# Performance work log

Hardware: AMD Instinct MI355X
Metric: run time of the kernel (lower is better)

Reference implementation:

```python
import jax, jax.numpy as jnp
import numpy as np

PATCH = 15  # box-filter kernel size (odd -> SAME padding == padding=PATCH//2, stride 1)


def _box_filter(x, k):
    """All-ones kxk conv2d, stride 1, zero pad k//2. x: (N,1,H,W).
    The ones kernel is separable: ones(k,k) = ones(k,1) @ ones(1,k)."""
    dn = ('NCHW', 'OIHW', 'NCHW')
    kh = jnp.ones((1, 1, k, 1), x.dtype)
    kw = jnp.ones((1, 1, 1, k), x.dtype)
    x = jax.lax.conv_general_dilated(x, kh, (1, 1), 'SAME', dimension_numbers=dn)
    x = jax.lax.conv_general_dilated(x, kw, (1, 1), 'SAME', dimension_numbers=dn)
    return x


def _rgb_to_yuv420(rgb):
    """rgb: (N,3,H,W) -> y:(N,H,W), u,v:(N,H/2,W/2) (2x2 avg-pooled chroma)."""
    r, g, b = rgb[:, 0], rgb[:, 1], rgb[:, 2]
    y = 0.299 * r + 0.587 * g + 0.114 * b
    u = -0.169 * r - 0.331 * g + 0.5 * b + 128.0
    v = 0.5 * r - 0.46 * g - 0.04 * b + 128.0
    n, h, w = u.shape
    u = u.reshape(n, h // 2, 2, w // 2, 2).mean(axis=(2, 4))
    v = v.reshape(n, h // 2, 2, w // 2, 2).mean(axis=(2, 4))
    return y, u, v


def _filtered_channels(img, k):
    y, u, v = _rgb_to_yuv420(img)
    return (_box_filter(y[:, None], k),
            _box_filter(u[:, None], k),
            _box_filter(v[:, None], k))


def setup_inputs() -> dict:
    key = jax.random.key(0)
    k1, k2 = jax.random.split(key)
    input_ = jax.random.uniform(k1, (16, 3, 512, 512), dtype=jnp.float32)
    target = jax.random.uniform(k2, (16, 3, 512, 512), dtype=jnp.float32)
    return {"input": input_, "target": target}


def reference(input, target):
    yi, ui, vi = _filtered_channels(input, PATCH)
    yt, ut, vt = _filtered_channels(target, PATCH)
    mse = lambda a, b: jnp.mean((a - b) ** 2)
    return mse(yi, yt) + mse(ui, ut) + mse(vi, vt)
```

## Files before the change

kernel.cpp:

```cpp
#include <hip/hip_runtime.h>

#define NIMG 16
#define H 512
#define W 512

__global__ __launch_bounds__(256, 4) void fused_wave_kernel(
        const float* __restrict__ in, const float* __restrict__ tgt,
        float invY, float invC, float* __restrict__ partials) {
    __shared__ float part[4];

    const int tid = threadIdx.x;
    const int wv  = tid >> 6;
    const int l   = tid & 63;

    const int g     = (blockIdx.x & 7) * 128 + (blockIdx.x >> 3);
    const int n     = g >> 6;
    const int band  = (g >> 2) & 15;
    const int strip = ((g & 3) << 2) | wv;

    const size_t plane = (size_t)H * W;
    const float* pi = in  + (size_t)n * 3 * plane;
    const float* pt = tgt + (size_t)n * 3 * plane;

    const int x  = (strip << 5) - 16 + l;
    const int xm = x < 0 ? 0 : (x > W - 1 ? W - 1 : x);
    const float mx = (x == xm) ? 1.f : 0.f;
    const float mL = (l >= 16 && l < 48) ? 1.f : 0.f;

    const bool ev = (l & 1) == 0;
    const float kr = ev ? -0.169f : 0.5f;
    const float kg = ev ? -0.331f : -0.46f;
    const float kb = ev ? 0.5f    : -0.04f;

    const int yBase = (band << 5) - 14;

    float ringA[8], ringB[8], ringC[16];
#pragma unroll
    for (int i = 0; i < 8; ++i) { ringA[i] = 0.f; ringB[i] = 0.f; }
#pragma unroll
    for (int i = 0; i < 16; ++i) ringC[i] = 0.f;

    float V = 0.f, Vc = 0.f, accY = 0.f, accC = 0.f;

#define PAIR(q) do {                                                          \
    const int yA = yBase + 2*(q), yB = yA + 1;                                \
    const int yAc = yA < 0 ? 0 : (yA > H-1 ? H-1 : yA);                       \
    const int yBc = yB < 0 ? 0 : (yB > H-1 ? H-1 : yB);                       \
    const float mA = (yA == yAc) ? mx : 0.f;                                  \
    const float mB = (yB == yBc) ? mx : 0.f;                                  \
    const size_t oA = (size_t)yAc * W + xm;                                   \
    const size_t oB = (size_t)yBc * W + xm;                                   \
    const float irA = pi[oA], igA = pi[plane+oA], ibA = pi[2*plane+oA];       \
    const float trA = pt[oA], tgA = pt[plane+oA], tbA = pt[2*plane+oA];       \
    const float irB = pi[oB], igB = pi[plane+oB], ibB = pi[2*plane+oB];       \
    const float trB = pt[oB], tgB = pt[plane+oB], tbB = pt[2*plane+oB];       \
    const float drA = (irA-trA)*mA, dgA = (igA-tgA)*mA, dbA = (ibA-tbA)*mA;   \
    const float drB = (irB-trB)*mB, dgB = (igB-tgB)*mB, dbB = (ibB-tbB)*mB;   \
    const float dYA = 0.299f*drA + 0.587f*dgA + 0.114f*dbA;                   \
    const float dYB = 0.299f*drB + 0.587f*dgB + 0.114f*dbB;                   \
    const float Va = V + dYA - ringB[(q) & 7];           \
    const float Vb = Va + dYB - ringA[((q)+1) & 7];      \
    ringA[(q) & 7] = dYA;                                                     \
    ringB[(q) & 7] = dYB;                                                     \
    V = Vb;                                                                   \
    if ((q) >= 10 && (q) <= 26) {             \
        float PA = Va, PB = Vb;                                               \
        _Pragma("unroll")                                                     \
        for (int d = 1; d <= 32; d <<= 1) {                                   \
            const float tA = __shfl_up(PA, d, 64);                            \
            const float tB = __shfl_up(PB, d, 64);                            \
            PA += (l >= d) ? tA : 0.f;                                        \
            PB += (l >= d) ? tB : 0.f;                                        \
        }                                                                     \
        const float hA = __shfl_down(PA, 7, 64) - __shfl_up(PA, 8, 64);       \
        const float hB = __shfl_down(PB, 7, 64) - __shfl_up(PB, 8, 64);       \
        if ((q) >= 11) accY += hA * hA * mL;        \
        if ((q) <= 25) accY += hB * hB * mL;        \
    }                                                                         \
    const float hr = drA + drB, hg = dgA + dgB, hb = dbA + dbB;               \
    const float sr = hr + __shfl_xor(hr, 1, 64);                              \
    const float sg = hg + __shfl_xor(hg, 1, 64);                              \
    const float sb = hb + __shfl_xor(hb, 1, 64);                              \
    const float Qc = (kr*sr + kg*sg + kb*sb) * 0.25f;                         \
    Vc += Qc - ringC[((q)+1) & 15];                                           \
    ringC[(q) & 15] = Qc;                                                     \
    if ((q) >= 14 && (q) <= 29) {                \
        float PC = Vc;                                                        \
        _Pragma("unroll")                                                     \
        for (int d = 2; d <= 32; d <<= 1) {                                   \
            const float tC = __shfl_up(PC, d, 64);                            \
            PC += (l >= d) ? tC : 0.f;                                        \
        }                                                                     \
        const float hc = __shfl_down(PC, 14, 64) - __shfl_up(PC, 16, 64);     \
        accC += hc * hc * mL;                                                 \
    }                                                                         \
} while (0)

    PAIR(0);  PAIR(1);  PAIR(2);  PAIR(3);  PAIR(4);  PAIR(5);
    PAIR(6);  PAIR(7);  PAIR(8);  PAIR(9);  PAIR(10); PAIR(11);
    PAIR(12); PAIR(13); PAIR(14); PAIR(15); PAIR(16); PAIR(17);
    PAIR(18); PAIR(19); PAIR(20); PAIR(21); PAIR(22); PAIR(23);
    PAIR(24); PAIR(25); PAIR(26); PAIR(27); PAIR(28); PAIR(29);
#undef PAIR

    float v = accY * invY + accC * invC;
    for (int o = 32; o > 0; o >>= 1) v += __shfl_down(v, o, 64);
    if (l == 0) part[wv] = v;
    __syncthreads();
    if (tid == 0)
        partials[blockIdx.x] = (part[0] + part[1]) + (part[2] + part[3]);
}

__global__ void final_reduce_kernel(const float* __restrict__ partials, int n,
                                    float* __restrict__ out) {
    float s = 0.f;
    for (int i = threadIdx.x; i < n; i += 256) s += partials[i];
    for (int o = 32; o > 0; o >>= 1) s += __shfl_down(s, o, 64);
    __shared__ float part[4];
    const int lane = threadIdx.x & 63, wid = threadIdx.x >> 6;
    if (lane == 0) part[wid] = s;
    __syncthreads();
    if (threadIdx.x == 0)
        *out = part[0] + part[1] + part[2] + part[3];
}

extern "C" void kernel_launch(void* const* d_in, const int* in_sizes, int n_in,
                              void* d_out, int out_size, void* d_ws, size_t ws_size,
                              hipStream_t stream) {
    const float* input  = (const float*)d_in[0];
    const float* target = (const float*)d_in[1];
    float* out = (float*)d_out;
    float* partials = (float*)d_ws;

    const float invY = 1.0f / (float)((size_t)NIMG * H * W);
    const float invC = 1.0f / (float)((size_t)NIMG * (H/2) * (W/2));

    fused_wave_kernel<<<1024, 256, 0, stream>>>(input, target, invY, invC, partials);
    final_reduce_kernel<<<1, 256, 0, stream>>>(partials, 1024, out);
}
```

Before: 139.9 us.

## Process two columns per lane with float2 loads, DPP scans and software prefetch

Each lane now handles two adjacent columns using float2 loads, so each wave covers a 64-column strip with less halo overhead, and the grid shrinks from 1024 to 512 blocks. The shuffle-based prefix scans are replaced with DPP row-shift scans plus ds_bpermute window extraction. Chroma is computed per lane directly from the pixel pair rather than through an xor shuffle. Loads for the next row pair are double-buffered ahead of consumption to hide memory latency. The cost is higher register pressure (launch bounds lowered to 2 blocks per CU) and half as many blocks, which may reduce occupancy.

```diff
diff --git a/kernel.cpp b/kernel.cpp
--- a/kernel.cpp
+++ b/kernel.cpp
@@ -4,7 +4,109 @@
 #define H 512
 #define W 512
 
-__global__ __launch_bounds__(256, 4) void fused_wave_kernel(
+
+template<int CTRL, int RM>
+static __device__ __forceinline__ float dppadd(float v) {
+    return v + __uint_as_float((unsigned)__builtin_amdgcn_update_dpp(
+        0, (int)__float_as_uint(v), CTRL, RM, 0xF, true));
+}
+
+static __device__ __forceinline__ float scan64(float v) {
+    v = dppadd<0x111, 0xF>(v);
+    v = dppadd<0x112, 0xF>(v);
+    v = dppadd<0x114, 0xF>(v);
+    v = dppadd<0x118, 0xF>(v);
+    v = dppadd<0x142, 0xA>(v);
+    v = dppadd<0x143, 0xC>(v);
+    return v;
+}
+
+static __device__ __forceinline__ float bpermf(int byteaddr, float v) {
+    return __uint_as_float((unsigned)__builtin_amdgcn_ds_bpermute(
+        byteaddr, (int)__float_as_uint(v)));
+}
+
+#define LOADP(q, S) do {                                                     \
+    const int yA_ = yBase + 2*(q);                                           \
+    const int yB_ = yA_ + 1;                                                 \
+    const int yAc_ = yA_ < 0 ? 0 : (yA_ > H-1 ? H-1 : yA_);                  \
+    const int yBc_ = yB_ < 0 ? 0 : (yB_ > H-1 ? H-1 : yB_);                  \
+    const size_t oA_ = (size_t)yAc_ * W + xcl;                               \
+    const size_t oB_ = (size_t)yBc_ * W + xcl;                               \
+    S##_0  = *(const float2*)(pi + oA_);                                     \
+    S##_1  = *(const float2*)(pi + plane + oA_);                             \
+    S##_2  = *(const float2*)(pi + 2*plane + oA_);                           \
+    S##_3  = *(const float2*)(pt + oA_);                                     \
+    S##_4  = *(const float2*)(pt + plane + oA_);                             \
+    S##_5  = *(const float2*)(pt + 2*plane + oA_);                           \
+    S##_6  = *(const float2*)(pi + oB_);                                     \
+    S##_7  = *(const float2*)(pi + plane + oB_);                             \
+    S##_8  = *(const float2*)(pi + 2*plane + oB_);                           \
+    S##_9  = *(const float2*)(pt + oB_);                                     \
+    S##_10 = *(const float2*)(pt + plane + oB_);                             \
+    S##_11 = *(const float2*)(pt + 2*plane + oB_);                           \
+} while (0)
+
+#define CONS(q, S) do {                                                      \
+    const int yA_ = yBase + 2*(q);                                           \
+    const float mA_ = ((unsigned)yA_       < (unsigned)H) ? mx : 0.f;        \
+    const float mB_ = ((unsigned)(yA_ + 1) < (unsigned)H) ? mx : 0.f;        \
+    const float drA0_ = (S##_0.x - S##_3.x) * mA_;                           \
+    const float drA1_ = (S##_0.y - S##_3.y) * mA_;                           \
+    const float dgA0_ = (S##_1.x - S##_4.x) * mA_;                           \
+    const float dgA1_ = (S##_1.y - S##_4.y) * mA_;                           \
+    const float dbA0_ = (S##_2.x - S##_5.x) * mA_;                           \
+    const float dbA1_ = (S##_2.y - S##_5.y) * mA_;                           \
+    const float drB0_ = (S##_6.x - S##_9.x) * mB_;                           \
+    const float drB1_ = (S##_6.y - S##_9.y) * mB_;                           \
+    const float dgB0_ = (S##_7.x - S##_10.x) * mB_;                          \
+    const float dgB1_ = (S##_7.y - S##_10.y) * mB_;                          \
+    const float dbB0_ = (S##_8.x - S##_11.x) * mB_;                          \
+    const float dbB1_ = (S##_8.y - S##_11.y) * mB_;                          \
+    const float dYA0_ = 0.299f*drA0_ + 0.587f*dgA0_ + 0.114f*dbA0_;          \
+    const float dYA1_ = 0.299f*drA1_ + 0.587f*dgA1_ + 0.114f*dbA1_;          \
+    const float dYB0_ = 0.299f*drB0_ + 0.587f*dgB0_ + 0.114f*dbB0_;          \
+    const float dYB1_ = 0.299f*drB1_ + 0.587f*dgB1_ + 0.114f*dbB1_;          \
+                    \
+    const float sr_ = (drA0_ + drA1_) + (drB0_ + drB1_);                     \
+    const float sg_ = (dgA0_ + dgA1_) + (dgB0_ + dgB1_);                     \
+    const float sb_ = (dbA0_ + dbA1_) + (dbB0_ + dbB1_);                     \
+    const float u_ = (-0.169f*sr_ - 0.331f*sg_ + 0.5f *sb_) * 0.25f;         \
+    const float w_ = ( 0.5f  *sr_ - 0.46f *sg_ - 0.04f*sb_) * 0.25f;         \
+         \
+    const float VA0_ = V0 + dYA0_ - rB0[(q) & 7];                            \
+    const float VB0_ = VA0_ + dYB0_ - rA0[((q)+1) & 7];                      \
+    rA0[(q) & 7] = dYA0_;  rB0[(q) & 7] = dYB0_;  V0 = VB0_;                 \
+    const float VA1_ = V1 + dYA1_ - rB1[(q) & 7];                            \
+    const float VB1_ = VA1_ + dYB1_ - rA1[((q)+1) & 7];                      \
+    rA1[(q) & 7] = dYA1_;  rB1[(q) & 7] = dYB1_;  V1 = VB1_;                 \
+    const float VU_ = CU + u_ - rU[((q)+1) & 15];                            \
+    rU[(q) & 15] = u_;  CU = VU_;                                            \
+    const float VV_ = CV + w_ - rV[((q)+1) & 15];                            \
+    rV[(q) & 15] = w_;  CV = VV_;                                            \
+        \
+    if ((q) >= 11 && (q) <= 26) {         \
+        const float SA_ = scan64(VA0_ + VA1_);                               \
+        const float h0_ = SA_ - VA1_ - bpermf(am8, SA_);                     \
+        const float h1_ = h0_ + VA1_ - bpermf(am7, VA0_);                    \
+        accY += (h0_ * h0_) * mH0 + (h1_ * h1_) * mH1;                       \
+    }                                                                        \
+    if ((q) >= 10 && (q) <= 25) {         \
+        const float SB_ = scan64(VB0_ + VB1_);                               \
+        const float h0_ = SB_ - VB1_ - bpermf(am8, SB_);                     \
+        const float h1_ = h0_ + VB1_ - bpermf(am7, VB0_);                    \
+        accY += (h0_ * h0_) * mH0 + (h1_ * h1_) * mH1;                       \
+    }                                                                        \
+    if ((q) >= 14) {                    \
+        const float SU_ = scan64(VU_);                                       \
+        const float hU_ = SU_ - bpermf(am15, SU_);                           \
+        const float SV_ = scan64(VV_);                                       \
+        const float hV_ = SV_ - bpermf(am15, SV_);                           \
+        accC += (hU_ * hU_ + hV_ * hV_) * mC;                                \
+    }                                                                        \
+} while (0)
+
+__global__ __launch_bounds__(256, 2) void fused_wave_kernel(
         const float* __restrict__ in, const float* __restrict__ tgt,
         float invY, float invC, float* __restrict__ partials) {
     __shared__ float part[4];
@@ -13,95 +115,59 @@
     const int wv  = tid >> 6;
     const int l   = tid & 63;
 
-    const int g     = (blockIdx.x & 7) * 128 + (blockIdx.x >> 3);
-    const int n     = g >> 6;
-    const int band  = (g >> 2) & 15;
-    const int strip = ((g & 3) << 2) | wv;
+    const int g     = (blockIdx.x & 7) * 64 + (blockIdx.x >> 3);
+    const int n     = g >> 5;
+    const int band  = (g >> 1) & 15;
+    const int strip = ((g & 1) << 2) | wv;
 
     const size_t plane = (size_t)H * W;
     const float* pi = in  + (size_t)n * 3 * plane;
     const float* pt = tgt + (size_t)n * 3 * plane;
 
-    const int x  = (strip << 5) - 16 + l;
-    const int xm = x < 0 ? 0 : (x > W - 1 ? W - 1 : x);
-    const float mx = (x == xm) ? 1.f : 0.f;
-    const float mL = (l >= 16 && l < 48) ? 1.f : 0.f;
-
-    const bool ev = (l & 1) == 0;
-    const float kr = ev ? -0.169f : 0.5f;
-    const float kg = ev ? -0.331f : -0.46f;
-    const float kb = ev ? 0.5f    : -0.04f;
-
-    const int yBase = (band << 5) - 14;
-
-    float ringA[8], ringB[8], ringC[16];
+    const int R0 = band << 5;
+    const int yBase = R0 - 14;
+
+    const int x0 = (strip << 6) - 32 + 2 * l;
+    const int xcl = x0 < 0 ? 0 : (x0 > W - 2 ? W - 2 : x0);
+    const float mx = (x0 == xcl) ? 1.f : 0.f;
+
+    const float mH0 = (l >= 20 && l <= 51) ? 1.f : 0.f;
+    const float mH1 = (l >= 19 && l <= 50) ? 1.f : 0.f;
+    const float mC  = (l >= 23 && l <= 54) ? 1.f : 0.f;
+
+    const int am8  = (l - 8)  << 2;
+    const int am7  = (l - 7)  << 2;
+    const int am15 = (l - 15) << 2;
+
+    float rA0[8], rA1[8], rB0[8], rB1[8], rU[16], rV[16];
 #pragma unroll
-    for (int i = 0; i < 8; ++i) { ringA[i] = 0.f; ringB[i] = 0.f; }
+    for (int i = 0; i < 8; ++i) { rA0[i] = 0.f; rA1[i] = 0.f; rB0[i] = 0.f; rB1[i] = 0.f; }
 #pragma unroll
-    for (int i = 0; i < 16; ++i) ringC[i] = 0.f;
-
-    float V = 0.f, Vc = 0.f, accY = 0.f, accC = 0.f;
-
-#define PAIR(q) do {                                                          \
-    const int yA = yBase + 2*(q), yB = yA + 1;                                \
-    const int yAc = yA < 0 ? 0 : (yA > H-1 ? H-1 : yA);                       \
-    const int yBc = yB < 0 ? 0 : (yB > H-1 ? H-1 : yB);                       \
-    const float mA = (yA == yAc) ? mx : 0.f;                                  \
-    const float mB = (yB == yBc) ? mx : 0.f;                                  \
-    const size_t oA = (size_t)yAc * W + xm;                                   \
-    const size_t oB = (size_t)yBc * W + xm;                                   \
-    const float irA = pi[oA], igA = pi[plane+oA], ibA = pi[2*plane+oA];       \
-    const float trA = pt[oA], tgA = pt[plane+oA], tbA = pt[2*plane+oA];       \
-    const float irB = pi[oB], igB = pi[plane+oB], ibB = pi[2*plane+oB];       \
-    const float trB = pt[oB], tgB = pt[plane+oB], tbB = pt[2*plane+oB];       \
-    const float drA = (irA-trA)*mA, dgA = (igA-tgA)*mA, dbA = (ibA-tbA)*mA;   \
-    const float drB = (irB-trB)*mB, dgB = (igB-tgB)*mB, dbB = (ibB-tbB)*mB;   \
-    const float dYA = 0.299f*drA + 0.587f*dgA + 0.114f*dbA;                   \
-    const float dYB = 0.299f*drB + 0.587f*dgB + 0.114f*dbB;                   \
-    const float Va = V + dYA - ringB[(q) & 7];           \
-    const float Vb = Va + dYB - ringA[((q)+1) & 7];      \
-    ringA[(q) & 7] = dYA;                                                     \
-    ringB[(q) & 7] = dYB;                                                     \
-    V = Vb;                                                                   \
-    if ((q) >= 10 && (q) <= 26) {             \
-        float PA = Va, PB = Vb;                                               \
-        _Pragma("unroll")                                                     \
-        for (int d = 1; d <= 32; d <<= 1) {                                   \
-            const float tA = __shfl_up(PA, d, 64);                            \
-            const float tB = __shfl_up(PB, d, 64);                            \
-            PA += (l >= d) ? tA : 0.f;                                        \
-            PB += (l >= d) ? tB : 0.f;                                        \
-        }                                                                     \
-        const float hA = __shfl_down(PA, 7, 64) - __shfl_up(PA, 8, 64);       \
-        const float hB = __shfl_down(PB, 7, 64) - __shfl_up(PB, 8, 64);       \
-        if ((q) >= 11) accY += hA * hA * mL;        \
-        if ((q) <= 25) accY += hB * hB * mL;        \
-    }                                                                         \
-    const float hr = drA + drB, hg = dgA + dgB, hb = dbA + dbB;               \
-    const float sr = hr + __shfl_xor(hr, 1, 64);                              \
-    const float sg = hg + __shfl_xor(hg, 1, 64);                              \
-    const float sb = hb + __shfl_xor(hb, 1, 64);                              \
-    const float Qc = (kr*sr + kg*sg + kb*sb) * 0.25f;                         \
-    Vc += Qc - ringC[((q)+1) & 15];                                           \
-    ringC[(q) & 15] = Qc;                                                     \
-    if ((q) >= 14 && (q) <= 29) {                \
-        float PC = Vc;                                                        \
-        _Pragma("unroll")                                                     \
-        for (int d = 2; d <= 32; d <<= 1) {                                   \
-            const float tC = __shfl_up(PC, d, 64);                            \
-            PC += (l >= d) ? tC : 0.f;                                        \
-        }                                                                     \
-        const float hc = __shfl_down(PC, 14, 64) - __shfl_up(PC, 16, 64);     \
-        accC += hc * hc * mL;                                                 \
-    }                                                                         \
-} while (0)
-
-    PAIR(0);  PAIR(1);  PAIR(2);  PAIR(3);  PAIR(4);  PAIR(5);
-    PAIR(6);  PAIR(7);  PAIR(8);  PAIR(9);  PAIR(10); PAIR(11);
-    PAIR(12); PAIR(13); PAIR(14); PAIR(15); PAIR(16); PAIR(17);
-    PAIR(18); PAIR(19); PAIR(20); PAIR(21); PAIR(22); PAIR(23);
-    PAIR(24); PAIR(25); PAIR(26); PAIR(27); PAIR(28); PAIR(29);
-#undef PAIR
+    for (int i = 0; i < 16; ++i) { rU[i] = 0.f; rV[i] = 0.f; }
+
+    float V0 = 0.f, V1 = 0.f, CU = 0.f, CV = 0.f;
+    float accY = 0.f, accC = 0.f;
+
+    float2 A_0,A_1,A_2,A_3,A_4,A_5,A_6,A_7,A_8,A_9,A_10,A_11;
+    float2 B_0,B_1,B_2,B_3,B_4,B_5,B_6,B_7,B_8,B_9,B_10,B_11;
+
+    LOADP(0, A);
+    LOADP(1, B);
+    CONS(0, A);  LOADP(2, A);   CONS(1, B);  LOADP(3, B);
+    CONS(2, A);  LOADP(4, A);   CONS(3, B);  LOADP(5, B);
+    CONS(4, A);  LOADP(6, A);   CONS(5, B);  LOADP(7, B);
+    CONS(6, A);  LOADP(8, A);   CONS(7, B);  LOADP(9, B);
+    CONS(8, A);  LOADP(10, A);  CONS(9, B);  LOADP(11, B);
+    CONS(10, A); LOADP(12, A);  CONS(11, B); LOADP(13, B);
+    CONS(12, A); LOADP(14, A);  CONS(13, B); LOADP(15, B);
+    CONS(14, A); LOADP(16, A);  CONS(15, B); LOADP(17, B);
+    CONS(16, A); LOADP(18, A);  CONS(17, B); LOADP(19, B);
+    CONS(18, A); LOADP(20, A);  CONS(19, B); LOADP(21, B);
+    CONS(20, A); LOADP(22, A);  CONS(21, B); LOADP(23, B);
+    CONS(22, A); LOADP(24, A);  CONS(23, B); LOADP(25, B);
+    CONS(24, A); LOADP(26, A);  CONS(25, B); LOADP(27, B);
+    CONS(26, A); LOADP(28, A);  CONS(27, B); LOADP(29, B);
+    CONS(28, A);                CONS(29, B);
 
     float v = accY * invY + accC * invC;
     for (int o = 32; o > 0; o >>= 1) v += __shfl_down(v, o, 64);
@@ -111,10 +177,10 @@
         partials[blockIdx.x] = (part[0] + part[1]) + (part[2] + part[3]);
 }
 
-__global__ void final_reduce_kernel(const float* __restrict__ partials, int n,
+__global__ void final_reduce_kernel(const float* __restrict__ partials, int np,
                                     float* __restrict__ out) {
     float s = 0.f;
-    for (int i = threadIdx.x; i < n; i += 256) s += partials[i];
+    for (int i = threadIdx.x; i < np; i += 256) s += partials[i];
     for (int o = 32; o > 0; o >>= 1) s += __shfl_down(s, o, 64);
     __shared__ float part[4];
     const int lane = threadIdx.x & 63, wid = threadIdx.x >> 6;
@@ -135,6 +201,6 @@
     const float invY = 1.0f / (float)((size_t)NIMG * H * W);
     const float invC = 1.0f / (float)((size_t)NIMG * (H/2) * (W/2));
 
-    fused_wave_kernel<<<1024, 256, 0, stream>>>(input, target, invY, invC, partials);
-    final_reduce_kernel<<<1, 256, 0, stream>>>(partials, 1024, out);
-}
+    fused_wave_kernel<<<512, 256, 0, stream>>>(input, target, invY, invC, partials);
+    final_reduce_kernel<<<1, 256, 0, stream>>>(partials, 512, out);
+}
```

Result: faster. 135.6 us (-3.1%).
